# Performance work log

Measured on AMD Instinct MI355X. Metric: run time of the kernel, lower is better.

Reference implementation:

```python
import jax, jax.numpy as jnp
import numpy as np

V, E, HID, K, S = 100000, 256, 512, 20, 4096
HD = HID // 2  # per-direction LSTM hidden
START_ID, STOP_ID = 18, 19


def setup_inputs() -> dict:
    key = jax.random.key(0)
    ks = jax.random.split(key, 14)
    sentence = jax.random.randint(ks[0], (S,), 0, V)
    tags = jax.random.randint(ks[1], (S,), 0, START_ID)  # real tags only
    embed = jax.random.normal(ks[2], (V, E), jnp.float32) * 0.1
    w_ih_f = jax.random.normal(ks[3], (4 * HD, E), jnp.float32) * 0.05
    w_hh_f = jax.random.normal(ks[4], (4 * HD, HD), jnp.float32) * 0.05
    b_f = jax.random.normal(ks[5], (4 * HD,), jnp.float32) * 0.05
    w_ih_b = jax.random.normal(ks[6], (4 * HD, E), jnp.float32) * 0.05
    w_hh_b = jax.random.normal(ks[7], (4 * HD, HD), jnp.float32) * 0.05
    b_b = jax.random.normal(ks[8], (4 * HD,), jnp.float32) * 0.05
    h0 = jax.random.normal(ks[9], (2, HD), jnp.float32)
    c0 = jax.random.normal(ks[10], (2, HD), jnp.float32)
    emit_W = jax.random.normal(ks[11], (K, HID), jnp.float32) * 0.05
    emit_b = jax.random.normal(ks[12], (K,), jnp.float32) * 0.05
    transition = jax.random.normal(ks[13], (K, K), jnp.float32)
    transition = transition.at[START_ID, :].set(-10000.0)
    transition = transition.at[:, STOP_ID].set(-10000.0)
    return dict(sentence=sentence, tags=tags, embed=embed,
                w_ih_f=w_ih_f, w_hh_f=w_hh_f, b_f=b_f,
                w_ih_b=w_ih_b, w_hh_b=w_hh_b, b_b=b_b,
                h0=h0, c0=c0, emit_W=emit_W, emit_b=emit_b,
                transition=transition)


def _lstm_scan(xs, w_ih, w_hh, b, h, c):
    # xs: (S, E); torch gate order i, f, g, o
    def step(carry, x):
        h, c = carry
        z = x @ w_ih.T + h @ w_hh.T + b  # (4*HD,)
        i, f, g, o = jnp.split(z, 4)
        i, f, o = jax.nn.sigmoid(i), jax.nn.sigmoid(f), jax.nn.sigmoid(o)
        g = jnp.tanh(g)
        c = f * c + i * g
        h = o * jnp.tanh(c)
        return (h, c), h
    _, hs = jax.lax.scan(step, (h, c), xs)
    return hs  # (S, HD)


def reference(sentence, tags, embed, w_ih_f, w_hh_f, b_f,
              w_ih_b, w_hh_b, b_b, h0, c0, emit_W, emit_b, transition):
    xs = embed[sentence]  # (S, E)
    h_fwd = _lstm_scan(xs, w_ih_f, w_hh_f, b_f, h0[0], c0[0])
    h_bwd = _lstm_scan(xs[::-1], w_ih_b, w_hh_b, b_b, h0[1], c0[1])[::-1]
    feats = jnp.concatenate([h_fwd, h_bwd], axis=-1) @ emit_W.T + emit_b  # (S, K)

    # CRF forward algorithm (log-partition), tag dim fully vectorized.
    init_fv = jnp.full((K,), -10000.0, feats.dtype).at[START_ID].set(0.0)

    def crf_step(fv, feat):
        # fv_new[next] = logsumexp_prev(fv[prev] + T[next, prev] + feat[next])
        fv = jax.scipy.special.logsumexp(fv[None, :] + transition + feat[:, None], axis=1)
        return fv, None

    fv, _ = jax.lax.scan(crf_step, init_fv, feats)
    log_z = jax.scipy.special.logsumexp(fv + transition[STOP_ID])

    # Gold path score.
    tags_ext = jnp.concatenate([jnp.array([START_ID], tags.dtype), tags])
    gold = (transition[tags_ext[1:], tags_ext[:-1]].sum()
            + feats[jnp.arange(S), tags].sum()
            + transition[STOP_ID, tags[-1]])
    return jnp.stack([log_z, gold])
```

## Files before the change

### kernel.cpp

```cpp
#include <hip/hip_runtime.h>
#include <stdint.h>

#define SLEN 4096
#define EDIM 256
#define HD 256
#define G4 1024
#define KT 20
#define START_ID 18
#define STOP_ID 19

#define NLC 9
#define HPAD 144
#define HBUF (4 * HPAD)
#define LSTM_LDS_BYTES (2048 + 1024 * NLC * 16)

typedef _Float16 half_t;
typedef _Float16 half2_t __attribute__((ext_vector_type(2)));

__device__ __forceinline__ float dot2(uint32_t w, uint32_t h, float acc) {
#if __has_builtin(__builtin_amdgcn_fdot2)
    return __builtin_amdgcn_fdot2(__builtin_bit_cast(half2_t, w),
                                  __builtin_bit_cast(half2_t, h), acc, false);
#else
    half2_t wv = __builtin_bit_cast(half2_t, w);
    half2_t hv = __builtin_bit_cast(half2_t, h);
    acc += (float)wv.x * (float)hv.x;
    acc += (float)wv.y * (float)hv.y;
    return acc;
#endif
}

__device__ __forceinline__ float fsig(float x) { return 1.f / (1.f + __expf(-x)); }
__device__ __forceinline__ float ftanh(float x) { return 1.f - 2.f / (__expf(2.f * x) + 1.f); }


__global__ __launch_bounds__(256) void k_transpose_ih(const float* __restrict__ wf,
                                                      const float* __restrict__ wb,
                                                      float* __restrict__ wT) {
    __shared__ float tile[32][33];
    int d = blockIdx.z;
    const float* w = d ? wb : wf;
    int ob = blockIdx.x * 32;
    int eb = blockIdx.y * 32;
    int tx = threadIdx.x & 31, ty = threadIdx.x >> 5;
#pragma unroll
    for (int r = 0; r < 32; r += 8)
        tile[ty + r][tx] = w[(long)(ob + ty + r) * EDIM + eb + tx];
    __syncthreads();
    float* dst = wT + (long)d * EDIM * G4;
#pragma unroll
    for (int r = 0; r < 32; r += 8)
        dst[(long)(eb + ty + r) * G4 + ob + tx] = tile[tx][ty + r];
}

__global__ __launch_bounds__(1024) void k_pack_hh(const float* __restrict__ whf,
                                                  const float* __restrict__ whb,
                                                  uint32_t* __restrict__ wpack,
                                                  uint32_t* __restrict__ wtail) {
    int d = blockIdx.y;
    const float* W = d ? whb : whf;
    int t = threadIdx.x;
    int l = t & 63;
    int w = t >> 6;
    int kq = l >> 4;
    int j = (w << 4) | (l & 15);
    int bx = blockIdx.x;

    auto packdw = [&](int dd) -> uint32_t {
        int cc = dd >> 2, qq = dd & 3;
        int gate = cc >> 3;
        int row = gate * 256 + j;
        int k = kq * 64 + (cc & 7) * 8 + qq * 2;
        half2_t p = {(half_t)W[(long)row * HD + k], (half_t)W[(long)row * HD + k + 1]};
        return __builtin_bit_cast(uint32_t, p);
    };

    if (bx < 92) {
        wpack[(d * 92 + bx) * 1024 + t] = packdw(bx);
    } else {
        int cb = bx - 92;
        uint4* dst = (uint4*)wtail;
        dst[(d * NLC + cb) * 1024 + t] = make_uint4(packdw(92 + cb * 4), packdw(93 + cb * 4),
                                                    packdw(94 + cb * 4), packdw(95 + cb * 4));
    }
}

__global__ __launch_bounds__(256) void k_zx(const int* __restrict__ sentence,
                                            const float* __restrict__ embed,
                                            const float* __restrict__ wT,
                                            const float* __restrict__ bf,
                                            const float* __restrict__ bb,
                                            float* __restrict__ zxp) {
    int d = blockIdx.y;
    int s0 = blockIdx.x * 16;
    const float* bias = d ? bb : bf;
    __shared__ float xbuf[16][EDIM];
    int u = threadIdx.x;
    for (int r = 0; r < 16; r++) {
        int row = sentence[s0 + r];
        xbuf[r][u] = embed[(long)row * EDIM + u];
    }
    __syncthreads();
    const float* wTd = wT + (long)d * EDIM * G4;
    float4 a[16];
    float4 bv = make_float4(bias[u], bias[256 + u], bias[512 + u], bias[768 + u]);
#pragma unroll
    for (int r = 0; r < 16; r++) a[r] = bv;
    for (int e = 0; e < EDIM; e += 4) {
        float w0[4], w1[4], w2[4], w3[4];
#pragma unroll
        for (int k = 0; k < 4; k++) {
            w0[k] = wTd[(long)(e + k) * G4 + u];
            w1[k] = wTd[(long)(e + k) * G4 + 256 + u];
            w2[k] = wTd[(long)(e + k) * G4 + 512 + u];
            w3[k] = wTd[(long)(e + k) * G4 + 768 + u];
        }
#pragma unroll
        for (int r = 0; r < 16; r++) {
            float4 x4 = *(const float4*)&xbuf[r][e];
            float xv[4] = {x4.x, x4.y, x4.z, x4.w};
#pragma unroll
            for (int k = 0; k < 4; k++) {
                a[r].x += w0[k] * xv[k];
                a[r].y += w1[k] * xv[k];
                a[r].z += w2[k] * xv[k];
                a[r].w += w3[k] * xv[k];
            }
        }
    }
#pragma unroll
    for (int r = 0; r < 16; r++)
        *(float4*)&zxp[(long)(d * SLEN + s0 + r) * G4 + u * 4] = a[r];
}

__global__ __launch_bounds__(1024, 4) void k_lstm(const float* __restrict__ zxp,
                                                  const uint32_t* __restrict__ wpack,
                                                  const uint4* __restrict__ wtail,
                                                  const float* __restrict__ h0,
                                                  const float* __restrict__ c0,
                                                  float* __restrict__ hs) {
    extern __shared__ char smem[];
    char* hbase = smem;
    uint4* tail = (uint4*)(smem + 2048);

    int d = blockIdx.x;
    int t = threadIdx.x;
    int l = t & 63;
    int w = t >> 6;
    int kq = l >> 4;
    int lj = l & 15;
    int j = (w << 4) | lj;

    uint32_t wreg[92];
#pragma unroll
    for (int kk = 0; kk < 92; kk++) wreg[kk] = wpack[(d * 92 + kk) * 1024 + t];

#pragma unroll
    for (int cb = 0; cb < NLC; cb++)
        tail[cb * 1024 + t] = wtail[(d * NLC + cb) * 1024 + t];

    float c = c0[d * HD + j];
    if (t < 128) {
        int u2 = 2 * t;
        half2_t p = {(half_t)h0[d * HD + u2], (half_t)h0[d * HD + u2 + 1]};
        *(uint32_t*)(hbase + (u2 >> 6) * HPAD + (u2 & 63) * 2) = __builtin_bit_cast(uint32_t, p);
    }
    __syncthreads();

    const float* zxd = zxp + (long)d * SLEN * G4;
    float* hsd = hs + (long)d * SLEN * HD + j;

    int sx0 = d ? (SLEN - 1) : 0;
    float4 zxn = *(const float4*)&zxd[(long)sx0 * G4 + j * 4];

    for (int s = 0; s < SLEN; s++) {
        const int p = s & 1;
        float4 zx = zxn;
        if (s + 1 < SLEN) {
            int sxn = d ? (SLEN - 2 - s) : (s + 1);
            zxn = *(const float4*)&zxd[(long)sxn * G4 + j * 4];
        }

        const uint4* hq = (const uint4*)(hbase + p * HBUF + kq * HPAD);
        float aI0 = 0.f, aI1 = 0.f, aF0 = 0.f, aF1 = 0.f;
        float aG0 = 0.f, aG1 = 0.f, aO0 = 0.f, aO1 = 0.f;
#pragma unroll
        for (int cc = 0; cc < 8; cc++) {
            uint4 hv = hq[cc];
            aI0 = dot2(wreg[4 * cc + 0], hv.x, aI0);
            aI1 = dot2(wreg[4 * cc + 1], hv.y, aI1);
            aI0 = dot2(wreg[4 * cc + 2], hv.z, aI0);
            aI1 = dot2(wreg[4 * cc + 3], hv.w, aI1);
            aF0 = dot2(wreg[32 + 4 * cc + 0], hv.x, aF0);
            aF1 = dot2(wreg[32 + 4 * cc + 1], hv.y, aF1);
            aF0 = dot2(wreg[32 + 4 * cc + 2], hv.z, aF0);
            aF1 = dot2(wreg[32 + 4 * cc + 3], hv.w, aF1);
            if (cc < 7) {
                aG0 = dot2(wreg[64 + 4 * cc + 0], hv.x, aG0);
                aG1 = dot2(wreg[64 + 4 * cc + 1], hv.y, aG1);
                aG0 = dot2(wreg[64 + 4 * cc + 2], hv.z, aG0);
                aG1 = dot2(wreg[64 + 4 * cc + 3], hv.w, aG1);
            } else {
                uint4 tw = tail[t];
                aG0 = dot2(tw.x, hv.x, aG0);
                aG1 = dot2(tw.y, hv.y, aG1);
                aG0 = dot2(tw.z, hv.z, aG0);
                aG1 = dot2(tw.w, hv.w, aG1);
            }
            uint4 ow = tail[(1 + cc) * 1024 + t];
            aO0 = dot2(ow.x, hv.x, aO0);
            aO1 = dot2(ow.y, hv.y, aO1);
            aO0 = dot2(ow.z, hv.z, aO0);
            aO1 = dot2(ow.w, hv.w, aO1);
        }

        float zi = aI0 + aI1, zf = aF0 + aF1, zg = aG0 + aG1, zo = aO0 + aO1;
        zi += __shfl_xor(zi, 16, 64);
        zf += __shfl_xor(zf, 16, 64);
        zg += __shfl_xor(zg, 16, 64);
        zo += __shfl_xor(zo, 16, 64);
        zi += __shfl_xor(zi, 32, 64);
        zf += __shfl_xor(zf, 32, 64);
        zg += __shfl_xor(zg, 32, 64);
        zo += __shfl_xor(zo, 32, 64);
        zi += zx.x; zf += zx.y; zg += zx.z; zo += zx.w;

        float ig = fsig(zi), fg = fsig(zf), og = fsig(zo);
        float gg = ftanh(zg);
        c = fg * c + ig * gg;
        float hval = og * ftanh(c);
        if (l < 16) {
            int sx = d ? (SLEN - 1 - s) : s;
            hsd[(long)sx * HD] = hval;
            *(half_t*)(hbase + (p ^ 1) * HBUF + (j >> 6) * HPAD + (j & 63) * 2) = (half_t)hval;
        }
        __syncthreads();
    }
}

__global__ __launch_bounds__(192) void k_feats(const float* __restrict__ hs,
                                               const float* __restrict__ emitW,
                                               const float* __restrict__ emitb,
                                               float* __restrict__ feats) {
    __shared__ float wb[KT][516];
    __shared__ float hb[8][516];
    int tid = threadIdx.x;
    int s0 = blockIdx.x * 8;
    for (int idx = tid; idx < KT * 512; idx += 192) {
        wb[idx >> 9][idx & 511] = emitW[idx];
    }
    for (int idx = tid; idx < 8 * 512; idx += 192) {
        int sl = idx >> 9, jj = idx & 511;
        float v = (jj < 256) ? hs[(long)(s0 + sl) * HD + jj]
                             : hs[(long)(SLEN + s0 + sl) * HD + (jj - 256)];
        hb[sl][jj] = v;
    }
    __syncthreads();
    if (tid < 160) {
        int sl = tid / KT, k = tid % KT;
        float acc = emitb[k];
        for (int jj = 0; jj < 512; jj += 4) {
            float4 wv = *(const float4*)&wb[k][jj];
            float4 hv = *(const float4*)&hb[sl][jj];
            acc += wv.x * hv.x + wv.y * hv.y + wv.z * hv.z + wv.w * hv.w;
        }
        feats[(long)(s0 + sl) * KT + k] = acc;
    }
}

__global__ __launch_bounds__(256) void k_gold(const float* __restrict__ feats,
                                              const int* __restrict__ tags,
                                              const float* __restrict__ trans,
                                              float* __restrict__ out) {
    __shared__ float red[256];
    int tid = threadIdx.x;
    float local = 0.f;
    for (int s2 = tid; s2 < SLEN; s2 += 256) {
        int cur = tags[s2];
        int prev = s2 ? tags[s2 - 1] : START_ID;
        local += trans[cur * KT + prev] + feats[(long)s2 * KT + cur];
    }
    red[tid] = local;
    __syncthreads();
    for (int off = 128; off; off >>= 1) {
        if (tid < off) red[tid] += red[tid + off];
        __syncthreads();
    }
    if (tid == 0) out[1] = red[0] + trans[STOP_ID * KT + tags[SLEN - 1]];
}

__global__ __launch_bounds__(512) void k_crf_chunk(const float* __restrict__ feats,
                                                   const float* __restrict__ trans,
                                                   float* __restrict__ mats) {
    __shared__ float T[KT][KT + 1];
    __shared__ float fb[16][KT];
    __shared__ float cur[2][KT][KT + 1];
    int tid = threadIdx.x;
    int t0 = blockIdx.x * 16;
    if (tid < KT * KT) T[tid / KT][tid % KT] = trans[tid];
    for (int idx = tid; idx < 16 * KT; idx += 512) fb[idx / KT][idx % KT] = feats[(long)t0 * KT + idx];
    __syncthreads();
    int i = tid / KT, jc = tid % KT;
    bool act = tid < KT * KT;
    if (act) cur[0][i][jc] = T[i][jc] + fb[0][i];
    __syncthreads();
    for (int m = 1; m < 16; m++) {
        int p = (m - 1) & 1;
        float nv = 0.f;
        if (act) {
            float vs[KT], vmax = -1e30f;
#pragma unroll
            for (int k = 0; k < KT; k++) { vs[k] = T[i][k] + cur[p][k][jc]; vmax = fmaxf(vmax, vs[k]); }
            float sum = 0.f;
#pragma unroll
            for (int k = 0; k < KT; k++) sum += __expf(vs[k] - vmax);
            nv = fb[m][i] + vmax + __logf(sum);
        }
        if (act) cur[p ^ 1][i][jc] = nv;
        __syncthreads();
    }
    if (act) mats[(long)blockIdx.x * (KT * KT) + tid] = cur[1][i][jc];
}

__global__ __launch_bounds__(512) void k_crf_combine(const float* __restrict__ in,
                                                     float* __restrict__ out_mats,
                                                     int per_block,
                                                     const float* __restrict__ trans,
                                                     float* __restrict__ d_out_ptr,
                                                     int finalize) {
    __shared__ float A[KT][KT + 1];
    __shared__ float cur[2][KT][KT + 1];
    int tid = threadIdx.x;
    int b = blockIdx.x;
    int i = tid / KT, jc = tid % KT;
    bool act = tid < KT * KT;
    const float* base = in + (long)b * per_block * (KT * KT);
    if (act) cur[0][i][jc] = base[tid];
    __syncthreads();
    for (int m = 1; m < per_block; m++) {
        int p = (m - 1) & 1;
        if (act) A[i][jc] = base[(long)m * KT * KT + tid];
        __syncthreads();
        float nv = 0.f;
        if (act) {
            float vs[KT], vmax = -1e30f;
#pragma unroll
            for (int k = 0; k < KT; k++) { vs[k] = A[i][k] + cur[p][k][jc]; vmax = fmaxf(vmax, vs[k]); }
            float sum = 0.f;
#pragma unroll
            for (int k = 0; k < KT; k++) sum += __expf(vs[k] - vmax);
            nv = vmax + __logf(sum);
        }
        if (act) cur[p ^ 1][i][jc] = nv;
        __syncthreads();
    }
    int fbuf = (per_block - 1) & 1;
    if (!finalize) {
        if (act) out_mats[(long)b * KT * KT + tid] = cur[fbuf][i][jc];
        return;
    }
    if (tid == 0) {
        float fv[KT];
        for (int ii = 0; ii < KT; ii++) {
            float vs[KT], vmax = -1e30f;
            for (int k = 0; k < KT; k++) {
                float v = cur[fbuf][ii][k] + (k == START_ID ? 0.f : -10000.f);
                vs[k] = v;
                vmax = fmaxf(vmax, v);
            }
            float sum = 0.f;
            for (int k = 0; k < KT; k++) sum += __expf(vs[k] - vmax);
            fv[ii] = vmax + __logf(sum);
        }
        float vs2[KT], vmax = -1e30f;
        for (int ii = 0; ii < KT; ii++) {
            float v = fv[ii] + trans[STOP_ID * KT + ii];
            vs2[ii] = v;
            vmax = fmaxf(vmax, v);
        }
        float sum = 0.f;
        for (int ii = 0; ii < KT; ii++) sum += __expf(vs2[ii] - vmax);
        d_out_ptr[0] = vmax + __logf(sum);
    }
}

extern "C" void kernel_launch(void* const* d_in, const int* in_sizes, int n_in,
                              void* d_out, int out_size, void* d_ws, size_t ws_size,
                              hipStream_t stream) {
    const int* sentence = (const int*)d_in[0];
    const int* tags = (const int*)d_in[1];
    const float* embed = (const float*)d_in[2];
    const float* w_ih_f = (const float*)d_in[3];
    const float* w_hh_f = (const float*)d_in[4];
    const float* b_f = (const float*)d_in[5];
    const float* w_ih_b = (const float*)d_in[6];
    const float* w_hh_b = (const float*)d_in[7];
    const float* b_b = (const float*)d_in[8];
    const float* h0 = (const float*)d_in[9];
    const float* c0 = (const float*)d_in[10];
    const float* emit_W = (const float*)d_in[11];
    const float* emit_b = (const float*)d_in[12];
    const float* transition = (const float*)d_in[13];
    float* out = (float*)d_out;

    char* ws = (char*)d_ws;
    float* zxp = (float*)(ws + 0);
    float* hs = (float*)(ws + 33554432);
    float* wT = (float*)(ws + 41943040);
    uint32_t* wpack = (uint32_t*)(ws + 44040192);
    uint32_t* wtail = (uint32_t*)(ws + 44793856);
    float* feats = (float*)(ws + 45088768);
    float* mats = (float*)(ws + 45416448);
    float* mats2 = (float*)(ws + 45826048);

    (void)hipFuncSetAttribute((const void*)k_lstm,
                              hipFuncAttributeMaxDynamicSharedMemorySize,
                              LSTM_LDS_BYTES);

    k_transpose_ih<<<dim3(32, 8, 2), 256, 0, stream>>>(w_ih_f, w_ih_b, wT);
    k_pack_hh<<<dim3(101, 2), 1024, 0, stream>>>(w_hh_f, w_hh_b, wpack, wtail);
    k_zx<<<dim3(256, 2), 256, 0, stream>>>(sentence, embed, wT, b_f, b_b, zxp);
    k_lstm<<<dim3(2), 1024, LSTM_LDS_BYTES, stream>>>(zxp, wpack, (const uint4*)wtail, h0, c0, hs);
    k_feats<<<dim3(512), 192, 0, stream>>>(hs, emit_W, emit_b, feats);
    k_gold<<<dim3(1), 256, 0, stream>>>(feats, tags, transition, out);
    k_crf_chunk<<<dim3(256), 512, 0, stream>>>(feats, transition, mats);
    k_crf_combine<<<dim3(16), 512, 0, stream>>>(mats, mats2, 16, transition, out, 0);
    k_crf_combine<<<dim3(1), 512, 0, stream>>>(mats2, nullptr, 16, transition, out, 1);
}
```

Measured before the change: 9.095 ms.

## Split each LSTM direction across two workgroups with flag-synchronized hidden-state exchange

The recurrent LSTM kernel now uses four workgroups instead of two, each owning half of a direction's hidden units. Every workgroup keeps all its recurrent weights in registers, which removes the LDS-resident weight tail. Each step, the partner's half of h is read from global memory after spinning on an agent-scope flag. Partial gate sums from the non-owned k-range are combined through LDS. This halves per-workgroup dot-product work, but adds a cross-workgroup global handshake on every step that may add latency to the serial chain. It also relies on both workgroups of a pair being resident at the same time.

```diff
diff --git a/kernel.cpp b/kernel.cpp
--- a/kernel.cpp
+++ b/kernel.cpp
@@ -8,11 +8,6 @@
 #define KT 20
 #define START_ID 18
 #define STOP_ID 19
-
-#define NLC 9
-#define HPAD 144
-#define HBUF (4 * HPAD)
-#define LSTM_LDS_BYTES (2048 + 1024 * NLC * 16)
 
 typedef _Float16 half_t;
 typedef _Float16 half2_t __attribute__((ext_vector_type(2)));
@@ -55,33 +50,29 @@
 
 __global__ __launch_bounds__(1024) void k_pack_hh(const float* __restrict__ whf,
                                                   const float* __restrict__ whb,
-                                                  uint32_t* __restrict__ wpack,
-                                                  uint32_t* __restrict__ wtail) {
-    int d = blockIdx.y;
+                                                  uint4* __restrict__ wpack,
+                                                  uint32_t* __restrict__ flags) {
+    int b = blockIdx.x;
+    int d = b >> 1, half = b & 1;
     const float* W = d ? whb : whf;
     int t = threadIdx.x;
-    int l = t & 63;
-    int w = t >> 6;
-    int kq = l >> 4;
-    int j = (w << 4) | (l & 15);
-    int bx = blockIdx.x;
-
-    auto packdw = [&](int dd) -> uint32_t {
-        int cc = dd >> 2, qq = dd & 3;
-        int gate = cc >> 3;
-        int row = gate * 256 + j;
-        int k = kq * 64 + (cc & 7) * 8 + qq * 2;
-        half2_t p = {(half_t)W[(long)row * HD + k], (half_t)W[(long)row * HD + k + 1]};
-        return __builtin_bit_cast(uint32_t, p);
-    };
-
-    if (bx < 92) {
-        wpack[(d * 92 + bx) * 1024 + t] = packdw(bx);
-    } else {
-        int cb = bx - 92;
-        uint4* dst = (uint4*)wtail;
-        dst[(d * NLC + cb) * 1024 + t] = make_uint4(packdw(92 + cb * 4), packdw(93 + cb * 4),
-                                                    packdw(94 + cb * 4), packdw(95 + cb * 4));
+    int l = t & 63, w = t >> 6;
+    int ju = ((w & 7) << 4) | (l & 15);
+    int kq = ((w >> 3) << 2) | (l >> 4);
+    if (b == 0 && t < 4) flags[t] = 0;
+#pragma unroll
+    for (int cc = 0; cc < 16; cc++) {
+        int g = cc >> 2, kc = cc & 3;
+        int row = g * 256 + half * 128 + ju;
+        int kb = kq * 32 + kc * 8;
+        uint32_t q[4];
+#pragma unroll
+        for (int dw = 0; dw < 4; dw++) {
+            half2_t p = {(half_t)W[(long)row * HD + kb + 2 * dw],
+                         (half_t)W[(long)row * HD + kb + 2 * dw + 1]};
+            q[dw] = __builtin_bit_cast(uint32_t, p);
+        }
+        wpack[(b * 16 + cc) * 1024 + t] = make_uint4(q[0], q[1], q[2], q[3]);
     }
 }
 
@@ -134,87 +125,97 @@
 }
 
 __global__ __launch_bounds__(1024, 4) void k_lstm(const float* __restrict__ zxp,
-                                                  const uint32_t* __restrict__ wpack,
-                                                  const uint4* __restrict__ wtail,
+                                                  const uint4* __restrict__ wpack,
                                                   const float* __restrict__ h0,
                                                   const float* __restrict__ c0,
-                                                  float* __restrict__ hs) {
-    extern __shared__ char smem[];
-    char* hbase = smem;
-    uint4* tail = (uint4*)(smem + 2048);
-
-    int d = blockIdx.x;
-    int t = threadIdx.x;
-    int l = t & 63;
-    int w = t >> 6;
-    int kq = l >> 4;
-    int lj = l & 15;
-    int j = (w << 4) | lj;
-
-    uint32_t wreg[92];
-#pragma unroll
-    for (int kk = 0; kk < 92; kk++) wreg[kk] = wpack[(d * 92 + kk) * 1024 + t];
-
-#pragma unroll
-    for (int cb = 0; cb < NLC; cb++)
-        tail[cb * 1024 + t] = wtail[(d * NLC + cb) * 1024 + t];
+                                                  float* __restrict__ hs,
+                                                  uint32_t* __restrict__ hx,
+                                                  uint32_t* __restrict__ flags) {
+    __shared__ __align__(16) half_t hfull[256];
+    __shared__ __align__(16) half_t hown[2][128];
+    __shared__ __align__(16) float zpart[128][4];
+
+    int b = blockIdx.x, d = b >> 1, half = b & 1;
+    int t = threadIdx.x, l = t & 63, w = t >> 6;
+    int kqg = w >> 3;
+    bool ownw = (kqg == half);
+    int ju = ((w & 7) << 4) | (l & 15);
+    int j = (half << 7) | ju;
+    int kq = (kqg << 2) | (l >> 4);
+
+    const uint4* wpd = wpack + (long)(b << 4) * 1024;
+    uint4 wreg[16];
+#pragma unroll
+    for (int cc = 0; cc < 16; cc++) wreg[cc] = wpd[cc * 1024 + t];
 
     float c = c0[d * HD + j];
     if (t < 128) {
-        int u2 = 2 * t;
-        half2_t p = {(half_t)h0[d * HD + u2], (half_t)h0[d * HD + u2 + 1]};
-        *(uint32_t*)(hbase + (u2 >> 6) * HPAD + (u2 & 63) * 2) = __builtin_bit_cast(uint32_t, p);
+        half2_t p0 = {(half_t)h0[d * HD + 2 * t], (half_t)h0[d * HD + 2 * t + 1]};
+        ((uint32_t*)hfull)[t] = __builtin_bit_cast(uint32_t, p0);
     }
     __syncthreads();
 
     const float* zxd = zxp + (long)d * SLEN * G4;
     float* hsd = hs + (long)d * SLEN * HD + j;
-
-    int sx0 = d ? (SLEN - 1) : 0;
-    float4 zxn = *(const float4*)&zxd[(long)sx0 * G4 + j * 4];
+    uint32_t* hx_mine = hx + b * 128;
+    const uint32_t* hx_part = hx + (b ^ 1) * 128;
+    uint32_t* mflag = flags + b;
+    uint32_t* pflag = flags + (b ^ 1);
+    const int pubw = half ? 7 : 15;
+
+    float4 zxn = make_float4(0.f, 0.f, 0.f, 0.f);
+    if (ownw) zxn = *(const float4*)&zxd[(long)(d ? SLEN - 1 : 0) * G4 + j * 4];
 
     for (int s = 0; s < SLEN; s++) {
         const int p = s & 1;
-        float4 zx = zxn;
-        if (s + 1 < SLEN) {
+        float4 zxq = zxn;
+        if (ownw && s + 1 < SLEN) {
             int sxn = d ? (SLEN - 2 - s) : (s + 1);
             zxn = *(const float4*)&zxd[(long)sxn * G4 + j * 4];
         }
 
-        const uint4* hq = (const uint4*)(hbase + p * HBUF + kq * HPAD);
-        float aI0 = 0.f, aI1 = 0.f, aF0 = 0.f, aF1 = 0.f;
-        float aG0 = 0.f, aG1 = 0.f, aO0 = 0.f, aO1 = 0.f;
-#pragma unroll
-        for (int cc = 0; cc < 8; cc++) {
-            uint4 hv = hq[cc];
-            aI0 = dot2(wreg[4 * cc + 0], hv.x, aI0);
-            aI1 = dot2(wreg[4 * cc + 1], hv.y, aI1);
-            aI0 = dot2(wreg[4 * cc + 2], hv.z, aI0);
-            aI1 = dot2(wreg[4 * cc + 3], hv.w, aI1);
-            aF0 = dot2(wreg[32 + 4 * cc + 0], hv.x, aF0);
-            aF1 = dot2(wreg[32 + 4 * cc + 1], hv.y, aF1);
-            aF0 = dot2(wreg[32 + 4 * cc + 2], hv.z, aF0);
-            aF1 = dot2(wreg[32 + 4 * cc + 3], hv.w, aF1);
-            if (cc < 7) {
-                aG0 = dot2(wreg[64 + 4 * cc + 0], hv.x, aG0);
-                aG1 = dot2(wreg[64 + 4 * cc + 1], hv.y, aG1);
-                aG0 = dot2(wreg[64 + 4 * cc + 2], hv.z, aG0);
-                aG1 = dot2(wreg[64 + 4 * cc + 3], hv.w, aG1);
-            } else {
-                uint4 tw = tail[t];
-                aG0 = dot2(tw.x, hv.x, aG0);
-                aG1 = dot2(tw.y, hv.y, aG1);
-                aG0 = dot2(tw.z, hv.z, aG0);
-                aG1 = dot2(tw.w, hv.w, aG1);
-            }
-            uint4 ow = tail[(1 + cc) * 1024 + t];
-            aO0 = dot2(ow.x, hv.x, aO0);
-            aO1 = dot2(ow.y, hv.y, aO1);
-            aO0 = dot2(ow.z, hv.z, aO0);
-            aO1 = dot2(ow.w, hv.w, aO1);
-        }
-
-        float zi = aI0 + aI1, zf = aF0 + aF1, zg = aG0 + aG1, zo = aO0 + aO1;
+        uint4 hv0, hv1, hv2, hv3;
+        if (s == 0) {
+            const char* hb = (const char*)hfull + (kq << 6);
+            hv0 = *(const uint4*)(hb);      hv1 = *(const uint4*)(hb + 16);
+            hv2 = *(const uint4*)(hb + 32); hv3 = *(const uint4*)(hb + 48);
+        } else if (ownw) {
+            const char* hb = (const char*)hown + p * 256 + ((l >> 4) << 6);
+            hv0 = *(const uint4*)(hb);      hv1 = *(const uint4*)(hb + 16);
+            hv2 = *(const uint4*)(hb + 32); hv3 = *(const uint4*)(hb + 48);
+        } else {
+            const uint32_t tgt = (uint32_t)s;
+            while (__hip_atomic_load(pflag, __ATOMIC_RELAXED, __HIP_MEMORY_SCOPE_AGENT) < tgt)
+                __builtin_amdgcn_s_sleep(2);
+            asm volatile("" ::: "memory");
+            const uint32_t* src = hx_part + p * 64 + ((l >> 4) << 4);
+            uint32_t hw[16];
+#pragma unroll
+            for (int q2 = 0; q2 < 16; q2++)
+                hw[q2] = __hip_atomic_load(src + q2, __ATOMIC_RELAXED, __HIP_MEMORY_SCOPE_AGENT);
+            hv0 = make_uint4(hw[0], hw[1], hw[2], hw[3]);
+            hv1 = make_uint4(hw[4], hw[5], hw[6], hw[7]);
+            hv2 = make_uint4(hw[8], hw[9], hw[10], hw[11]);
+            hv3 = make_uint4(hw[12], hw[13], hw[14], hw[15]);
+        }
+
+        float a0 = 0.f, b0 = 0.f, a1 = 0.f, b1 = 0.f;
+        float a2 = 0.f, b2 = 0.f, a3 = 0.f, b3 = 0.f;
+#define DOT4(kc, HV)                                                      \
+        a0 = dot2(wreg[kc].x, HV.x, a0);      b0 = dot2(wreg[kc].y, HV.y, b0);      \
+        a0 = dot2(wreg[kc].z, HV.z, a0);      b0 = dot2(wreg[kc].w, HV.w, b0);      \
+        a1 = dot2(wreg[4 + kc].x, HV.x, a1);  b1 = dot2(wreg[4 + kc].y, HV.y, b1);  \
+        a1 = dot2(wreg[4 + kc].z, HV.z, a1);  b1 = dot2(wreg[4 + kc].w, HV.w, b1);  \
+        a2 = dot2(wreg[8 + kc].x, HV.x, a2);  b2 = dot2(wreg[8 + kc].y, HV.y, b2);  \
+        a2 = dot2(wreg[8 + kc].z, HV.z, a2);  b2 = dot2(wreg[8 + kc].w, HV.w, b2);  \
+        a3 = dot2(wreg[12 + kc].x, HV.x, a3); b3 = dot2(wreg[12 + kc].y, HV.y, b3); \
+        a3 = dot2(wreg[12 + kc].z, HV.z, a3); b3 = dot2(wreg[12 + kc].w, HV.w, b3);
+        DOT4(0, hv0)
+        DOT4(1, hv1)
+        DOT4(2, hv2)
+        DOT4(3, hv3)
+#undef DOT4
+        float zi = a0 + b0, zf = a1 + b1, zg = a2 + b2, zo = a3 + b3;
         zi += __shfl_xor(zi, 16, 64);
         zf += __shfl_xor(zf, 16, 64);
         zg += __shfl_xor(zg, 16, 64);
@@ -223,18 +224,39 @@
         zf += __shfl_xor(zf, 32, 64);
         zg += __shfl_xor(zg, 32, 64);
         zo += __shfl_xor(zo, 32, 64);
-        zi += zx.x; zf += zx.y; zg += zx.z; zo += zx.w;
-
-        float ig = fsig(zi), fg = fsig(zf), og = fsig(zo);
-        float gg = ftanh(zg);
-        c = fg * c + ig * gg;
-        float hval = og * ftanh(c);
-        if (l < 16) {
-            int sx = d ? (SLEN - 1 - s) : s;
-            hsd[(long)sx * HD] = hval;
-            *(half_t*)(hbase + (p ^ 1) * HBUF + (j >> 6) * HPAD + (j & 63) * 2) = (half_t)hval;
-        }
-        __syncthreads();
+
+        if (!ownw && (l >> 4) == 0)
+            *(float4*)&zpart[ju][0] = make_float4(zi, zf, zg, zo);
+        __syncthreads();
+
+        if (ownw) {
+            float4 zp = *(const float4*)&zpart[ju][0];
+            float Zi = zi + zp.x + zxq.x;
+            float Zf = zf + zp.y + zxq.y;
+            float Zg = zg + zp.z + zxq.z;
+            float Zo = zo + zp.w + zxq.w;
+            float ig = fsig(Zi), fg = fsig(Zf), og = fsig(Zo);
+            float gg = ftanh(Zg);
+            c = fg * c + ig * gg;
+            float hval = og * ftanh(c);
+            if ((l >> 4) == 0) {
+                int sx = d ? (SLEN - 1 - s) : s;
+                hsd[(long)sx * HD] = hval;
+                hown[p ^ 1][ju] = (half_t)hval;
+            }
+        }
+        __syncthreads();
+
+        if (w == pubw && s + 1 < SLEN) {
+            if (l < 16) {
+                uint4 v = *(const uint4*)((const char*)hown + (p ^ 1) * 256 + l * 16);
+                *(uint4*)(hx_mine + (p ^ 1) * 64 + l * 4) = v;
+            }
+            __threadfence();
+            if (l == 0)
+                __hip_atomic_store(mflag, (uint32_t)(s + 1), __ATOMIC_RELEASE,
+                                   __HIP_MEMORY_SCOPE_AGENT);
+        }
     }
 }
 
@@ -407,20 +429,17 @@
     float* zxp = (float*)(ws + 0);
     float* hs = (float*)(ws + 33554432);
     float* wT = (float*)(ws + 41943040);
-    uint32_t* wpack = (uint32_t*)(ws + 44040192);
-    uint32_t* wtail = (uint32_t*)(ws + 44793856);
+    uint4* wpack = (uint4*)(ws + 44040192);
     float* feats = (float*)(ws + 45088768);
     float* mats = (float*)(ws + 45416448);
     float* mats2 = (float*)(ws + 45826048);
-
-    (void)hipFuncSetAttribute((const void*)k_lstm,
-                              hipFuncAttributeMaxDynamicSharedMemorySize,
-                              LSTM_LDS_BYTES);
+    uint32_t* hx = (uint32_t*)(ws + 45851648);
+    uint32_t* flags = (uint32_t*)(ws + 45855744);
 
     k_transpose_ih<<<dim3(32, 8, 2), 256, 0, stream>>>(w_ih_f, w_ih_b, wT);
-    k_pack_hh<<<dim3(101, 2), 1024, 0, stream>>>(w_hh_f, w_hh_b, wpack, wtail);
+    k_pack_hh<<<dim3(4), 1024, 0, stream>>>(w_hh_f, w_hh_b, wpack, flags);
     k_zx<<<dim3(256, 2), 256, 0, stream>>>(sentence, embed, wT, b_f, b_b, zxp);
-    k_lstm<<<dim3(2), 1024, LSTM_LDS_BYTES, stream>>>(zxp, wpack, (const uint4*)wtail, h0, c0, hs);
+    k_lstm<<<dim3(4), 1024, 0, stream>>>(zxp, wpack, h0, c0, hs, hx, flags);
     k_feats<<<dim3(512), 192, 0, stream>>>(hs, emit_W, emit_b, feats);
     k_gold<<<dim3(1), 256, 0, stream>>>(feats, tags, transition, out);
     k_crf_chunk<<<dim3(256), 512, 0, stream>>>(feats, transition, mats);
```

Result: no change. 9.001 ms (-1.0%).
